# Kernel optimization log

Hardware: AMD Instinct MI355X
Metric: run time of the kernel (lower is better)

The kernel has to match this reference:

```python
import jax, jax.numpy as jnp
import numpy as np

HEADS = 4
DIM_HEAD = 32


def setup_inputs() -> dict:
    key = jax.random.key(0)
    k1, k2, k3, k4 = jax.random.split(key, 4)
    dim = 256
    hidden = HEADS * DIM_HEAD  # 128
    x = jax.random.normal(k1, (4, dim, 64, 64), dtype=jnp.float32)
    # 1x1 convs are channel-mixing matmuls; store weights as [out_ch, in_ch]
    w_qkv = jax.random.normal(k2, (3 * hidden, dim), dtype=jnp.float32) * (dim ** -0.5)
    w_out = jax.random.normal(k3, (dim, hidden), dtype=jnp.float32) * (hidden ** -0.5)
    b_out = jax.random.normal(k4, (dim,), dtype=jnp.float32) * 0.02
    return {"x": x, "w_qkv": w_qkv, "w_out": w_out, "b_out": b_out}


def reference(x, w_qkv, w_out, b_out):
    b, c, h, w = x.shape
    n = h * w
    scale = DIM_HEAD ** -0.5
    xf = x.reshape(b, c, n)                                   # b c n
    qkv = jnp.einsum('oc,bcn->bon', w_qkv, xf)                # b (3*H*D) n
    q, k, v = jnp.split(qkv, 3, axis=1)                       # each b (H*D) n
    q = q.reshape(b, HEADS, DIM_HEAD, n) * scale              # b h d n
    k = k.reshape(b, HEADS, DIM_HEAD, n)
    v = v.reshape(b, HEADS, DIM_HEAD, n)
    sim = jnp.einsum('bhdi,bhdj->bhij', q, k)                 # b h n n
    attn = jax.nn.softmax(sim, axis=-1)                       # stable max-subtract inside
    out = jnp.einsum('bhij,bhdj->bhdi', attn, v)              # b h d n
    out = out.reshape(b, HEADS * DIM_HEAD, n)                 # b (h d) n
    out = jnp.einsum('oc,bcn->bon', w_out, out) + b_out[None, :, None]
    return out.reshape(b, -1, h, w)
```

## Files before the change

kernel.cpp:

```cpp
#include <hip/hip_runtime.h>
#include <hip/hip_bf16.h>
#include <stdint.h>

#define B_SZ 4
#define C_IN 256
#define N_SP 4096
#define HEADS 4
#define DH 32
#define HID 128

#define BI 128
#define BJ 64
#define PP 68

typedef short short4v __attribute__((ext_vector_type(4)));
typedef short short8 __attribute__((ext_vector_type(8)));
typedef float f32x4 __attribute__((ext_vector_type(4)));

#if __has_builtin(__builtin_amdgcn_exp2f)
#define EXP2 __builtin_amdgcn_exp2f
#else
#define EXP2 exp2f
#endif

__device__ __forceinline__ short f2bfs(float f) {
  return (short)((__float_as_uint(f) + 0x8000u) >> 16);
}
__device__ __forceinline__ uint32_t pk_bf(float a, float b) {
  uint32_t ua = __float_as_uint(a) + 0x8000u;
  uint32_t ub = __float_as_uint(b) + 0x8000u;
  return (ua >> 16) | (ub & 0xffff0000u);
}
__device__ __forceinline__ short8 ld_frag(const short* p) {
  short4v a = *(const short4v*)p;
  short4v b = *(const short4v*)(p + 4);
  return __builtin_shufflevector(a, b, 0, 1, 2, 3, 4, 5, 6, 7);
}
__device__ __forceinline__ f32x4 mfma16(short8 a, short8 b, f32x4 c) {
  return __builtin_amdgcn_mfma_f32_16x16x32_bf16(a, b, c, 0, 0, 0);
}

__global__ __launch_bounds__(256) void qkv_proj_k(
    const float* __restrict__ x, const float* __restrict__ w,
    float* __restrict__ qkf, short* __restrict__ vt) {
  const int t = threadIdx.x;
  const int n0 = blockIdx.x * 1024 + t * 4;
  const int o0 = blockIdx.y * 8;
  const int b = blockIdx.z;
  const float* xb = x + (size_t)b * C_IN * N_SP + n0;
  float acc[8][4];
#pragma unroll
  for (int r = 0; r < 8; ++r)
#pragma unroll
    for (int j = 0; j < 4; ++j) acc[r][j] = 0.f;
  for (int c = 0; c < C_IN; c += 2) {
    const float4 xa = *(const float4*)(xb + (size_t)c * N_SP);
    const float4 xc = *(const float4*)(xb + (size_t)(c + 1) * N_SP);
    const float xaj[4] = {xa.x, xa.y, xa.z, xa.w};
    const float xcj[4] = {xc.x, xc.y, xc.z, xc.w};
#pragma unroll
    for (int r = 0; r < 8; ++r) {
      const float2 wv = *(const float2*)(w + (size_t)(o0 + r) * C_IN + c);
#pragma unroll
      for (int j = 0; j < 4; ++j) acc[r][j] += wv.x * xaj[j] + wv.y * xcj[j];
    }
  }
  if (o0 < 256) {
    float* dst = qkf + ((size_t)b * 256 + o0) * N_SP + n0;
#pragma unroll
    for (int r = 0; r < 8; ++r)
      *(float4*)(dst + (size_t)r * N_SP) =
          make_float4(acc[r][0], acc[r][1], acc[r][2], acc[r][3]);
  } else {
    const int d0 = o0 & 31, h = (o0 >> 5) & 3;
    const int bh = b * HEADS + h;
#pragma unroll
    for (int r = 0; r < 8; ++r) {
      short4v p;
#pragma unroll
      for (int j = 0; j < 4; ++j) p[j] = f2bfs(acc[r][j]);
      *(short4v*)(vt + ((size_t)bh * DH + d0 + r) * N_SP + n0) = p;
    }
  }
}

__global__ __launch_bounds__(256) void qk_t_k(
    const float* __restrict__ qkf, short* __restrict__ qt, short* __restrict__ kt) {
  __shared__ short T[256 * 36];
  const int t = threadIdx.x;
  const int ntile = blockIdx.x, bh = blockIdx.y, z = blockIdx.z;
  const int b = bh >> 2, h = bh & 3;
  const float sc = z ? 1.f : (0.17677669529663687f * 1.4426950408889634f);
  const float* src = qkf + ((size_t)(b * 256 + z * 128 + h * 32)) * N_SP + ntile * 256;
  {
    const int d = t >> 3, m = t & 7;
    const float* sp = src + (size_t)d * N_SP + m * 32;
#pragma unroll
    for (int k2 = 0; k2 < 8; ++k2) {
      const float4 v = *(const float4*)(sp + k2 * 4);
      const int n = m * 32 + k2 * 4;
      T[(n + 0) * 36 + d] = f2bfs(v.x * sc);
      T[(n + 1) * 36 + d] = f2bfs(v.y * sc);
      T[(n + 2) * 36 + d] = f2bfs(v.z * sc);
      T[(n + 3) * 36 + d] = f2bfs(v.w * sc);
    }
  }
  __syncthreads();
  short* dst = (z ? kt : qt) + ((size_t)bh * N_SP + ntile * 256) * DH;
  const int ch = t & 3, nb = t >> 2;
#pragma unroll
  for (int rep = 0; rep < 4; ++rep) {
    const int n = rep * 64 + nb;
    const uint2 a = *(const uint2*)&T[n * 36 + ch * 8];
    const uint2 c = *(const uint2*)&T[n * 36 + ch * 8 + 4];
    uint4 o; o.x = a.x; o.y = a.y; o.z = c.x; o.w = c.y;
    *(uint4*)(dst + (size_t)n * DH + ch * 8) = o;
  }
}

__global__ __launch_bounds__(256, 2) void attn_k(
    const short* __restrict__ qt, const short* __restrict__ kt,
    const short* __restrict__ vt, float* __restrict__ att) {
  __shared__ short Ps[BI * PP];
  __shared__ float Osh[DH * 132];
  const int t = threadIdx.x;
  const int lane = t & 63, w = t >> 6;
  const int l15 = lane & 15, quad = lane >> 4;
  const int i0 = blockIdx.x * BI;
  const int bh = blockIdx.y;
  const short* qg = qt + ((size_t)bh * N_SP + i0) * DH;
  const short* kg = kt + (size_t)bh * N_SP * DH;
  const short* vg = vt + (size_t)bh * DH * N_SP;

  short8 bq[2];
#pragma unroll
  for (int tt = 0; tt < 2; ++tt)
    bq[tt] = *(const short8*)(qg + (size_t)(w * 32 + tt * 16 + l15) * DH + quad * 8);

  const f32x4 zz = {0.f, 0.f, 0.f, 0.f};
  f32x4 o_acc[2][2] = {{zz, zz}, {zz, zz}};
  float lsum[2] = {0.f, 0.f};
  short* prow[2];
#pragma unroll
  for (int tt = 0; tt < 2; ++tt) prow[tt] = Ps + (w * 32 + tt * 16 + l15) * PP;

  short8 akA[4], akB[4], vbA[2][2], vbB[2][2];
#pragma unroll
  for (int jt = 0; jt < 4; ++jt)
    akA[jt] = *(const short8*)(kg + (size_t)(jt * 16 + l15) * DH + quad * 8);
#pragma unroll
  for (int dt = 0; dt < 2; ++dt)
#pragma unroll
    for (int kk = 0; kk < 2; ++kk)
      vbA[dt][kk] = *(const short8*)(vg + (size_t)(dt * 16 + l15) * N_SP + kk * 32 + quad * 8);

  auto body = [&](const short8 (&akc)[4], const short8 (&vbc)[2][2],
                  short8 (&akn)[4], short8 (&vbn)[2][2], int jn) {
    f32x4 sf[2][4];
#pragma unroll
    for (int tt = 0; tt < 2; ++tt)
#pragma unroll
      for (int jt = 0; jt < 4; ++jt) sf[tt][jt] = mfma16(akc[jt], bq[tt], zz);
#pragma unroll
    for (int jt = 0; jt < 4; ++jt)
      akn[jt] = *(const short8*)(kg + (size_t)(jn + jt * 16 + l15) * DH + quad * 8);
#pragma unroll
    for (int dt = 0; dt < 2; ++dt)
#pragma unroll
      for (int kk = 0; kk < 2; ++kk)
        vbn[dt][kk] = *(const short8*)(vg + (size_t)(dt * 16 + l15) * N_SP + jn + kk * 32 + quad * 8);
#pragma unroll
    for (int tt = 0; tt < 2; ++tt)
#pragma unroll
      for (int jt = 0; jt < 4; ++jt) {
        const float e0 = EXP2(sf[tt][jt][0]);
        const float e1 = EXP2(sf[tt][jt][1]);
        const float e2 = EXP2(sf[tt][jt][2]);
        const float e3 = EXP2(sf[tt][jt][3]);
        lsum[tt] += (e0 + e1) + (e2 + e3);
        uint2 pk; pk.x = pk_bf(e0, e1); pk.y = pk_bf(e2, e3);
        *(uint2*)(prow[tt] + jt * 16 + quad * 4) = pk;
      }
    asm volatile("s_waitcnt lgkmcnt(0)" ::: "memory");
    short8 pa[2][2];
#pragma unroll
    for (int tt = 0; tt < 2; ++tt)
#pragma unroll
      for (int kk = 0; kk < 2; ++kk) pa[tt][kk] = ld_frag(prow[tt] + kk * 32 + quad * 8);
#pragma unroll
    for (int tt = 0; tt < 2; ++tt)
#pragma unroll
      for (int dt = 0; dt < 2; ++dt) {
        o_acc[tt][dt] = mfma16(pa[tt][0], vbc[dt][0], o_acc[tt][dt]);
        o_acc[tt][dt] = mfma16(pa[tt][1], vbc[dt][1], o_acc[tt][dt]);
      }
  };

  for (int jt0 = 0; jt0 < N_SP; jt0 += 2 * BJ) {
    body(akA, vbA, akB, vbB, (jt0 + BJ) & (N_SP - 1));
    body(akB, vbB, akA, vbA, (jt0 + 2 * BJ) & (N_SP - 1));
  }

#pragma unroll
  for (int tt = 0; tt < 2; ++tt) {
    lsum[tt] += __shfl_xor(lsum[tt], 16);
    lsum[tt] += __shfl_xor(lsum[tt], 32);
  }
  float linv[2][4];
#pragma unroll
  for (int tt = 0; tt < 2; ++tt)
#pragma unroll
    for (int r = 0; r < 4; ++r) linv[tt][r] = 1.f / __shfl(lsum[tt], quad * 4 + r);
#pragma unroll
  for (int tt = 0; tt < 2; ++tt)
#pragma unroll
    for (int dt = 0; dt < 2; ++dt)
#pragma unroll
      for (int r = 0; r < 4; ++r)
        Osh[(dt * 16 + l15) * 132 + w * 32 + tt * 16 + quad * 4 + r] =
            o_acc[tt][dt][r] * linv[tt][r];
  __syncthreads();
  {
    const int d = t >> 3, ch = t & 7;
    float* dst = att + ((size_t)bh * DH + d) * N_SP + i0 + ch * 16;
    const float* src = Osh + d * 132 + ch * 16;
#pragma unroll
    for (int k2 = 0; k2 < 4; ++k2) *(float4*)(dst + k2 * 4) = *(const float4*)(src + k2 * 4);
  }
}

__global__ __launch_bounds__(256) void out_proj_k(
    const float* __restrict__ att, const float* __restrict__ w,
    const float* __restrict__ bias, float* __restrict__ out) {
  const int t = threadIdx.x;
  const int n0 = blockIdx.x * 1024 + t * 4;
  const int o0 = blockIdx.y * 8;
  const int b = blockIdx.z;
  const float* ab = att + (size_t)b * HID * N_SP + n0;
  float acc[8][4];
#pragma unroll
  for (int r = 0; r < 8; ++r)
#pragma unroll
    for (int j = 0; j < 4; ++j) acc[r][j] = 0.f;
  for (int c = 0; c < HID; c += 2) {
    const float4 a0 = *(const float4*)(ab + (size_t)c * N_SP);
    const float4 a1 = *(const float4*)(ab + (size_t)(c + 1) * N_SP);
    const float a0j[4] = {a0.x, a0.y, a0.z, a0.w};
    const float a1j[4] = {a1.x, a1.y, a1.z, a1.w};
#pragma unroll
    for (int r = 0; r < 8; ++r) {
      const float2 wv = *(const float2*)(w + (size_t)(o0 + r) * HID + c);
#pragma unroll
      for (int j = 0; j < 4; ++j) acc[r][j] += wv.x * a0j[j] + wv.y * a1j[j];
    }
  }
#pragma unroll
  for (int r = 0; r < 8; ++r) {
    const float bv = bias[o0 + r];
    *(float4*)(out + ((size_t)b * C_IN + o0 + r) * N_SP + n0) =
        make_float4(acc[r][0] + bv, acc[r][1] + bv, acc[r][2] + bv, acc[r][3] + bv);
  }
}

extern "C" void kernel_launch(void* const* d_in, const int* in_sizes, int n_in,
                              void* d_out, int out_size, void* d_ws, size_t ws_size,
                              hipStream_t stream) {
  const float* x = (const float*)d_in[0];
  const float* w_qkv = (const float*)d_in[1];
  const float* w_out = (const float*)d_in[2];
  const float* b_out = (const float*)d_in[3];
  float* out = (float*)d_out;

  short* qt = (short*)d_ws;
  short* kt = qt + (size_t)16 * N_SP * DH;
  short* vt = kt + (size_t)16 * N_SP * DH;
  float* qkf = (float*)(vt + (size_t)16 * N_SP * DH);
  float* att = qkf;

  qkv_proj_k<<<dim3(4, 48, B_SZ), 256, 0, stream>>>(x, w_qkv, qkf, vt);
  qk_t_k<<<dim3(16, 16, 2), 256, 0, stream>>>(qkf, qt, kt);
  attn_k<<<dim3(N_SP / BI, B_SZ * HEADS), 256, 0, stream>>>(qt, kt, vt, att);
  out_proj_k<<<dim3(4, 32, B_SZ), 256, 0, stream>>>(att, w_out, b_out, out);
}
```

Before: 238.4 us.

## Split attention over two key halves and fuse Q/K transpose into projection

Splits the attention key range into two halves along a new grid dimension, so the attention launch has twice as many blocks, and raises the occupancy hint to 4 blocks per SM. Each half writes unnormalized partial outputs and row sums, and the output projection combines the halves and normalizes before the channel mix. The Q/K transpose to bf16 is folded into the projection kernel through shared memory, which removes the separate transpose kernel and the fp32 intermediate. The cost is extra partial-output traffic and more loads in the output projection. Softmax stays correct because exponent scaling is shared across halves, so no running max is needed.

```diff
diff --git a/kernel.cpp b/kernel.cpp
--- a/kernel.cpp
+++ b/kernel.cpp
@@ -11,6 +11,7 @@
 
 #define BI 128
 #define BJ 64
+#define JH 2048
 #define PP 68
 
 typedef short short4v __attribute__((ext_vector_type(4)));
@@ -42,11 +43,13 @@
 
 __global__ __launch_bounds__(256) void qkv_proj_k(
     const float* __restrict__ x, const float* __restrict__ w,
-    float* __restrict__ qkf, short* __restrict__ vt) {
+    short* __restrict__ qt, short* __restrict__ kt, short* __restrict__ vt) {
+  __shared__ short T2[DH * 260];
   const int t = threadIdx.x;
-  const int n0 = blockIdx.x * 1024 + t * 4;
-  const int o0 = blockIdx.y * 8;
-  const int b = blockIdx.z;
+  const int tn = t & 63, tr = t >> 6;
+  const int nb = blockIdx.x, og = blockIdx.y, b = blockIdx.z;
+  const int n0 = nb * 256 + tn * 4;
+  const int r0 = og * 32 + tr * 8;
   const float* xb = x + (size_t)b * C_IN * N_SP + n0;
   float acc[8][4];
 #pragma unroll
@@ -60,20 +63,14 @@
     const float xcj[4] = {xc.x, xc.y, xc.z, xc.w};
 #pragma unroll
     for (int r = 0; r < 8; ++r) {
-      const float2 wv = *(const float2*)(w + (size_t)(o0 + r) * C_IN + c);
+      const float2 wv = *(const float2*)(w + (size_t)(r0 + r) * C_IN + c);
 #pragma unroll
       for (int j = 0; j < 4; ++j) acc[r][j] += wv.x * xaj[j] + wv.y * xcj[j];
     }
   }
-  if (o0 < 256) {
-    float* dst = qkf + ((size_t)b * 256 + o0) * N_SP + n0;
-#pragma unroll
-    for (int r = 0; r < 8; ++r)
-      *(float4*)(dst + (size_t)r * N_SP) =
-          make_float4(acc[r][0], acc[r][1], acc[r][2], acc[r][3]);
-  } else {
-    const int d0 = o0 & 31, h = (o0 >> 5) & 3;
-    const int bh = b * HEADS + h;
+  const int sect = og >> 2, h = og & 3;
+  const int bh = b * HEADS + h, d0 = tr * 8;
+  if (sect == 2) {
 #pragma unroll
     for (int r = 0; r < 8; ++r) {
       short4v p;
@@ -81,53 +78,40 @@
       for (int j = 0; j < 4; ++j) p[j] = f2bfs(acc[r][j]);
       *(short4v*)(vt + ((size_t)bh * DH + d0 + r) * N_SP + n0) = p;
     }
-  }
-}
-
-__global__ __launch_bounds__(256) void qk_t_k(
-    const float* __restrict__ qkf, short* __restrict__ qt, short* __restrict__ kt) {
-  __shared__ short T[256 * 36];
-  const int t = threadIdx.x;
-  const int ntile = blockIdx.x, bh = blockIdx.y, z = blockIdx.z;
-  const int b = bh >> 2, h = bh & 3;
-  const float sc = z ? 1.f : (0.17677669529663687f * 1.4426950408889634f);
-  const float* src = qkf + ((size_t)(b * 256 + z * 128 + h * 32)) * N_SP + ntile * 256;
-  {
-    const int d = t >> 3, m = t & 7;
-    const float* sp = src + (size_t)d * N_SP + m * 32;
-#pragma unroll
-    for (int k2 = 0; k2 < 8; ++k2) {
-      const float4 v = *(const float4*)(sp + k2 * 4);
-      const int n = m * 32 + k2 * 4;
-      T[(n + 0) * 36 + d] = f2bfs(v.x * sc);
-      T[(n + 1) * 36 + d] = f2bfs(v.y * sc);
-      T[(n + 2) * 36 + d] = f2bfs(v.z * sc);
-      T[(n + 3) * 36 + d] = f2bfs(v.w * sc);
-    }
-  }
-  __syncthreads();
-  short* dst = (z ? kt : qt) + ((size_t)bh * N_SP + ntile * 256) * DH;
-  const int ch = t & 3, nb = t >> 2;
-#pragma unroll
-  for (int rep = 0; rep < 4; ++rep) {
-    const int n = rep * 64 + nb;
-    const uint2 a = *(const uint2*)&T[n * 36 + ch * 8];
-    const uint2 c = *(const uint2*)&T[n * 36 + ch * 8 + 4];
-    uint4 o; o.x = a.x; o.y = a.y; o.z = c.x; o.w = c.y;
-    *(uint4*)(dst + (size_t)n * DH + ch * 8) = o;
-  }
-}
-
-__global__ __launch_bounds__(256, 2) void attn_k(
+  } else {
+    const float sc = sect ? 1.f : (0.17677669529663687f * 1.4426950408889634f);
+#pragma unroll
+    for (int r = 0; r < 8; ++r) {
+      short4v p;
+#pragma unroll
+      for (int j = 0; j < 4; ++j) p[j] = f2bfs(acc[r][j] * sc);
+      *(short4v*)(T2 + (d0 + r) * 260 + tn * 4) = p;
+    }
+    __syncthreads();
+    short* dst = (sect ? kt : qt) + ((size_t)bh * N_SP + nb * 256) * DH;
+#pragma unroll
+    for (int k = 0; k < 4; ++k) {
+      const int g = t + 256 * k;
+      const int n = g >> 2, dq = g & 3;
+      short8 v;
+#pragma unroll
+      for (int e = 0; e < 8; ++e) v[e] = T2[(dq * 8 + e) * 260 + n];
+      *(short8*)(dst + (size_t)g * 8) = v;
+    }
+  }
+}
+
+__global__ __launch_bounds__(256, 4) void attn_k(
     const short* __restrict__ qt, const short* __restrict__ kt,
-    const short* __restrict__ vt, float* __restrict__ att) {
+    const short* __restrict__ vt, float* __restrict__ Oh, float* __restrict__ lg) {
   __shared__ short Ps[BI * PP];
   __shared__ float Osh[DH * 132];
   const int t = threadIdx.x;
   const int lane = t & 63, w = t >> 6;
   const int l15 = lane & 15, quad = lane >> 4;
   const int i0 = blockIdx.x * BI;
-  const int bh = blockIdx.y;
+  const int bh = blockIdx.y, jh = blockIdx.z;
+  const int jbeg = jh * JH;
   const short* qg = qt + ((size_t)bh * N_SP + i0) * DH;
   const short* kg = kt + (size_t)bh * N_SP * DH;
   const short* vg = vt + (size_t)bh * DH * N_SP;
@@ -147,12 +131,12 @@
   short8 akA[4], akB[4], vbA[2][2], vbB[2][2];
 #pragma unroll
   for (int jt = 0; jt < 4; ++jt)
-    akA[jt] = *(const short8*)(kg + (size_t)(jt * 16 + l15) * DH + quad * 8);
+    akA[jt] = *(const short8*)(kg + (size_t)(jbeg + jt * 16 + l15) * DH + quad * 8);
 #pragma unroll
   for (int dt = 0; dt < 2; ++dt)
 #pragma unroll
     for (int kk = 0; kk < 2; ++kk)
-      vbA[dt][kk] = *(const short8*)(vg + (size_t)(dt * 16 + l15) * N_SP + kk * 32 + quad * 8);
+      vbA[dt][kk] = *(const short8*)(vg + (size_t)(dt * 16 + l15) * N_SP + jbeg + kk * 32 + quad * 8);
 
   auto body = [&](const short8 (&akc)[4], const short8 (&vbc)[2][2],
                   short8 (&akn)[4], short8 (&vbn)[2][2], int jn) {
@@ -196,9 +180,9 @@
       }
   };
 
-  for (int jt0 = 0; jt0 < N_SP; jt0 += 2 * BJ) {
-    body(akA, vbA, akB, vbB, (jt0 + BJ) & (N_SP - 1));
-    body(akB, vbB, akA, vbA, (jt0 + 2 * BJ) & (N_SP - 1));
+  for (int off = 0; off < JH; off += 2 * BJ) {
+    body(akA, vbA, akB, vbB, jbeg + ((off + BJ) & (JH - 1)));
+    body(akB, vbB, akA, vbA, jbeg + ((off + 2 * BJ) & (JH - 1)));
   }
 
 #pragma unroll
@@ -206,23 +190,22 @@
     lsum[tt] += __shfl_xor(lsum[tt], 16);
     lsum[tt] += __shfl_xor(lsum[tt], 32);
   }
-  float linv[2][4];
+  if (quad == 0) {
+    float* lgp = lg + ((size_t)jh * 16 + bh) * N_SP + i0;
+    lgp[w * 32 + l15] = lsum[0];
+    lgp[w * 32 + 16 + l15] = lsum[1];
+  }
 #pragma unroll
   for (int tt = 0; tt < 2; ++tt)
 #pragma unroll
-    for (int r = 0; r < 4; ++r) linv[tt][r] = 1.f / __shfl(lsum[tt], quad * 4 + r);
-#pragma unroll
-  for (int tt = 0; tt < 2; ++tt)
-#pragma unroll
     for (int dt = 0; dt < 2; ++dt)
 #pragma unroll
       for (int r = 0; r < 4; ++r)
-        Osh[(dt * 16 + l15) * 132 + w * 32 + tt * 16 + quad * 4 + r] =
-            o_acc[tt][dt][r] * linv[tt][r];
+        Osh[(dt * 16 + l15) * 132 + w * 32 + tt * 16 + quad * 4 + r] = o_acc[tt][dt][r];
   __syncthreads();
   {
     const int d = t >> 3, ch = t & 7;
-    float* dst = att + ((size_t)bh * DH + d) * N_SP + i0 + ch * 16;
+    float* dst = Oh + ((size_t)jh * 512 + bh * DH + d) * N_SP + i0 + ch * 16;
     const float* src = Osh + d * 132 + ch * 16;
 #pragma unroll
     for (int k2 = 0; k2 < 4; ++k2) *(float4*)(dst + k2 * 4) = *(const float4*)(src + k2 * 4);
@@ -230,23 +213,38 @@
 }
 
 __global__ __launch_bounds__(256) void out_proj_k(
-    const float* __restrict__ att, const float* __restrict__ w,
-    const float* __restrict__ bias, float* __restrict__ out) {
+    const float* __restrict__ Oh, const float* __restrict__ lg,
+    const float* __restrict__ w, const float* __restrict__ bias,
+    float* __restrict__ out) {
   const int t = threadIdx.x;
   const int n0 = blockIdx.x * 1024 + t * 4;
   const int o0 = blockIdx.y * 8;
   const int b = blockIdx.z;
-  const float* ab = att + (size_t)b * HID * N_SP + n0;
+  const float* O0 = Oh + (size_t)(b * HID) * N_SP;
+  const float* O1 = O0 + (size_t)512 * N_SP;
+  float inv[4][4];
+#pragma unroll
+  for (int h = 0; h < 4; ++h) {
+    const float4 a = *(const float4*)(lg + (size_t)(b * 4 + h) * N_SP + n0);
+    const float4 c = *(const float4*)(lg + (size_t)(16 + b * 4 + h) * N_SP + n0);
+    inv[h][0] = 1.f / (a.x + c.x); inv[h][1] = 1.f / (a.y + c.y);
+    inv[h][2] = 1.f / (a.z + c.z); inv[h][3] = 1.f / (a.w + c.w);
+  }
   float acc[8][4];
 #pragma unroll
   for (int r = 0; r < 8; ++r)
 #pragma unroll
     for (int j = 0; j < 4; ++j) acc[r][j] = 0.f;
   for (int c = 0; c < HID; c += 2) {
-    const float4 a0 = *(const float4*)(ab + (size_t)c * N_SP);
-    const float4 a1 = *(const float4*)(ab + (size_t)(c + 1) * N_SP);
-    const float a0j[4] = {a0.x, a0.y, a0.z, a0.w};
-    const float a1j[4] = {a1.x, a1.y, a1.z, a1.w};
+    const int h = c >> 5;
+    const float4 p0 = *(const float4*)(O0 + (size_t)c * N_SP + n0);
+    const float4 q0 = *(const float4*)(O1 + (size_t)c * N_SP + n0);
+    const float4 p1 = *(const float4*)(O0 + (size_t)(c + 1) * N_SP + n0);
+    const float4 q1 = *(const float4*)(O1 + (size_t)(c + 1) * N_SP + n0);
+    float a0j[4] = {(p0.x + q0.x) * inv[h][0], (p0.y + q0.y) * inv[h][1],
+                    (p0.z + q0.z) * inv[h][2], (p0.w + q0.w) * inv[h][3]};
+    float a1j[4] = {(p1.x + q1.x) * inv[h][0], (p1.y + q1.y) * inv[h][1],
+                    (p1.z + q1.z) * inv[h][2], (p1.w + q1.w) * inv[h][3]};
 #pragma unroll
     for (int r = 0; r < 8; ++r) {
       const float2 wv = *(const float2*)(w + (size_t)(o0 + r) * HID + c);
@@ -274,11 +272,10 @@
   short* qt = (short*)d_ws;
   short* kt = qt + (size_t)16 * N_SP * DH;
   short* vt = kt + (size_t)16 * N_SP * DH;
-  float* qkf = (float*)(vt + (size_t)16 * N_SP * DH);
-  float* att = qkf;
-
-  qkv_proj_k<<<dim3(4, 48, B_SZ), 256, 0, stream>>>(x, w_qkv, qkf, vt);
-  qk_t_k<<<dim3(16, 16, 2), 256, 0, stream>>>(qkf, qt, kt);
-  attn_k<<<dim3(N_SP / BI, B_SZ * HEADS), 256, 0, stream>>>(qt, kt, vt, att);
-  out_proj_k<<<dim3(4, 32, B_SZ), 256, 0, stream>>>(att, w_out, b_out, out);
-}
+  float* Oh = (float*)(vt + (size_t)16 * N_SP * DH);
+  float* lg = Oh + (size_t)2 * 512 * N_SP;
+
+  qkv_proj_k<<<dim3(16, 12, B_SZ), 256, 0, stream>>>(x, w_qkv, qt, kt, vt);
+  attn_k<<<dim3(N_SP / BI, 16, 2), 256, 0, stream>>>(qt, kt, vt, Oh, lg);
+  out_proj_k<<<dim3(4, 32, B_SZ), 256, 0, stream>>>(Oh, lg, w_out, b_out, out);
+}
```

New measurement: 413.3 us. 1.73x slower.
